# Kernel tuning notes

Hardware: AMD Instinct MI355X
Metric: run time of the kernel (lower is better)

The kernel has to match this reference:

```python
import jax, jax.numpy as jnp
import numpy as np

SIGNAL_SIZE = 33554432  # 2**25
N_ELEMENTS = 25         # log2(SIGNAL_SIZE)


def fft_shift(a, shift):
    # Faithful port of the torch fft_shift (note: 'shift' variable is reused
    # in the original; the phase ramp overwrites it after shift_samples).
    shift = 1.0 - shift
    n_samples = a.shape[-1]
    shift_samples = shift * n_samples * 0.5
    spec = jnp.fft.rfft(a, norm='ortho')
    n_coeffs = spec.shape[-1]
    phase = jnp.arange(n_coeffs) * (2j * np.pi / n_coeffs)  # complex64 ramp
    spec = spec * jnp.exp(phase * shift_samples)
    return jnp.fft.irfft(spec, n=n_samples, norm='ortho')


def setup_inputs() -> dict:
    key = jax.random.key(0)
    elements = jax.random.uniform(key, (N_ELEMENTS,), minval=-1.0, maxval=1.0,
                                  dtype=jnp.float32)
    return {"elements": elements}


def reference(elements):
    # dirac impulse of size 2 at position 0
    signal = jnp.zeros(2, dtype=jnp.float32).at[0].set(1.0)
    for i in range(N_ELEMENTS):  # fixed trip count; sizes double each step
        if i > 0:
            new_signal = jnp.zeros(signal.shape[-1] * 2, dtype=signal.dtype)
            signal = new_signal.at[::2].set(signal)
        shift_factor = 1.0 / (2 ** i)
        signal = fft_shift(signal, elements[i] * shift_factor)
    return signal  # shape [SIGNAL_SIZE]
```

## Files before the change

### kernel.cpp

```cpp
#include <hip/hip_runtime.h>


constexpr float TWOPI_F = 6.28318530717958647692f;
constexpr unsigned M24 = 1u << 24;

__device__ __forceinline__ void phase_sincos(float th, float* sn, float* cs) {
    double d = (double)th * 0.15915494309189533577;
    d -= rint(d);
    float r = (float)d;
    *sn = __builtin_amdgcn_sinf(r);
    *cs = __builtin_amdgcn_cosf(r);
}

__device__ __forceinline__ void sincos_rev(float rev, float* sn, float* cs) {
    float r = rev - rintf(rev);
    *sn = __builtin_amdgcn_sinf(r);
    *cs = __builtin_amdgcn_cosf(r);
}

__device__ __forceinline__ float2 cmul(float2 a, float2 f) {
    return make_float2(a.x * f.x - a.y * f.y, a.x * f.y + a.y * f.x);
}
__device__ __forceinline__ float2 caddf(float2 a, float2 b) { return make_float2(a.x + b.x, a.y + b.y); }
__device__ __forceinline__ float2 csubf(float2 a, float2 b) { return make_float2(a.x - b.x, a.y - b.y); }
__device__ __forceinline__ float2 cmulw(float2 a, float c, float s) {
    return make_float2(a.x * c - a.y * s, a.x * s + a.y * c);
}

__device__ __forceinline__ int xcd_swizzle(int b, int nblocks) {
    int chunk = nblocks >> 3;
    return (b & 7) * chunk + (b >> 3);
}

__device__ __forceinline__ void fft16_inv(float2* v) {
    const float C1 = 0.92387953251128675613f;
    const float S1 = 0.38268343236508977173f;
    const float R2 = 0.70710678118654752440f;
    float2 h[16];
#pragma unroll
    for (int b = 0; b < 4; ++b) {
        float2 s02 = caddf(v[b], v[b + 8]);
        float2 d02 = csubf(v[b], v[b + 8]);
        float2 s13 = caddf(v[b + 4], v[b + 12]);
        float2 d13 = csubf(v[b + 4], v[b + 12]);
        float2 id13 = make_float2(-d13.y, d13.x);
        h[4 * b + 0] = caddf(s02, s13);
        h[4 * b + 1] = caddf(d02, id13);
        h[4 * b + 2] = csubf(s02, s13);
        h[4 * b + 3] = csubf(d02, id13);
    }
    h[5]  = cmulw(h[5],  C1,  S1);
    h[6]  = make_float2(R2 * (h[6].x - h[6].y),  R2 * (h[6].x + h[6].y));
    h[7]  = cmulw(h[7],  S1,  C1);
    h[9]  = make_float2(R2 * (h[9].x - h[9].y),  R2 * (h[9].x + h[9].y));
    h[10] = make_float2(-h[10].y, h[10].x);
    h[11] = cmulw(h[11], -R2, R2);
    h[13] = cmulw(h[13], S1,  C1);
    h[14] = cmulw(h[14], -R2, R2);
    h[15] = cmulw(h[15], -C1, -S1);
#pragma unroll
    for (int K1 = 0; K1 < 4; ++K1) {
        float2 a = h[K1], bb = h[4 + K1], cc = h[8 + K1], dd = h[12 + K1];
        float2 sac = caddf(a, cc), dac = csubf(a, cc);
        float2 sbd = caddf(bb, dd), dbd = csubf(bb, dd);
        float2 idbd = make_float2(-dbd.y, dbd.x);
        v[K1]      = caddf(sac, sbd);
        v[K1 + 4]  = caddf(dac, idbd);
        v[K1 + 8]  = csubf(sac, sbd);
        v[K1 + 12] = csubf(dac, idbd);
    }
}

__device__ __forceinline__ void ztwiddle(float2* v, int q) {
    float ss, cc;
    sincos_rev((float)q * (1.0f / 256.0f), &ss, &cc);
    float2 w = make_float2(1.0f, 0.0f), stp = make_float2(cc, ss);
#pragma unroll
    for (int K1 = 0; K1 < 16; ++K1) {
        v[K1] = cmul(v[K1], w);
        w = cmul(w, stp);
    }
}

__global__ __launch_bounds__(256) void build_q(const float* __restrict__ el,
                                               float2* __restrict__ Q) {
    __shared__ float c_s[18], s_s[18], T_s[18];
    int tid = threadIdx.x;
    if (tid < 18) {
        float e = el[tid];
        float shift1 = e * (1.0f / (float)(1u << tid));
        float sh2 = 1.0f - shift1;
        float s = sh2 * (float)(1u << tid);
        float c = (float)(6.2831853071795864769 / (double)((1u << tid) + 1u));
        c_s[tid] = c;
        s_s[tid] = s;
        float p  = (float)(1u << tid) * c;
        float th = p * s;
        float sn, cs; phase_sincos(th, &sn, &cs);
        T_s[tid] = cs;
    }
    __syncthreads();

    unsigned r = blockIdx.x * 256u + (unsigned)tid;
    if (r == 0u) { Q[0] = make_float2(1.0f, 0.0f); return; }

    unsigned t = (unsigned)__builtin_ctz(r);
    float Pr = T_s[t], Pi = 0.0f;

#pragma unroll
    for (int i = 1; i <= 17; ++i) {
        unsigned hi = 1u << i;
        int sd = (int)((r + hi) & (2u * hi - 1u)) - (int)hi;
        int K  = (i <= (int)t) ? 0 : (sd < 0 ? -sd : sd);
        float sgn = (sd < 0) ? -1.0f : 1.0f;
        float p  = (float)K * c_s[i];
        float th = p * s_s[i];
        float sn, cs; phase_sincos(th, &sn, &cs);
        float ssn = sgn * sn;
        float nr = Pr * cs - Pi * ssn;
        float ni = Pr * ssn + Pi * cs;
        Pr = nr; Pi = ni;
    }
    Q[r] = make_float2(Pr, Pi);
}

__device__ __forceinline__ float2 chain_factor(int i, unsigned k,
                                               const float* __restrict__ c_s,
                                               const float* __restrict__ s_s) {
    unsigned hi = 1u << i;
    int sd = (int)((k + hi) & (2u * hi - 1u)) - (int)hi;
    int K  = (sd < 0) ? -sd : sd;
    float sgn = (sd < 0) ? -1.0f : 1.0f;
    float p  = (float)K * c_s[i];
    float th = p * s_s[i];
    float sn, cs; phase_sincos(th, &sn, &cs);
    return make_float2(cs, sgn * sn);
}

struct WPair { float2 wk, wmk; };

__device__ __forceinline__ WPair chain_tail(unsigned k, float Pr, float Pi,
                                            const float* __restrict__ c_s,
                                            const float* __restrict__ s_s) {
    const float sc = 1.0f / 33554432.0f;
    unsigned mk = M24 - k;
    float thk = ((float)k  * c_s[24]) * s_s[24];
    float thm = ((float)mk * c_s[24]) * s_s[24];
    float snk, csk, snm, csm;
    phase_sincos(thk, &snk, &csk);
    phase_sincos(thm, &snm, &csm);

    float Skr = Pr * csk - Pi * snk;
    float Ski = Pr * snk + Pi * csk;
    float Smr = Pr * csm + Pi * snm;
    float Smi = Pr * snm - Pi * csm;

    float Ar = Skr + Smr, Ai = Ski - Smi;
    float Br = Skr - Smr, Bi = Ski + Smi;
    float ts, tc;
    sincos_rev((float)k * (1.0f / 33554432.0f), &ts, &tc);
    float Cr = tc * Br - ts * Bi;
    float Ci = ts * Br + tc * Bi;

    WPair w;
    w.wk  = make_float2((Ar - Ci) * sc, (Ai + Cr) * sc);
    w.wmk = make_float2((Ar + Ci) * sc, (Cr - Ai) * sc);
    return w;
}

__device__ __forceinline__ WPair chain_W(unsigned k,
                                         const float* __restrict__ c_s,
                                         const float* __restrict__ s_s,
                                         const float* __restrict__ T_s,
                                         const float2* __restrict__ Q) {
    unsigned t = (unsigned)__builtin_ctz(k);
    unsigned r = k & 0x3FFFFu;
    float Pr, Pi;
    if (r != 0u) {
        float2 q = Q[r];
        Pr = q.x; Pi = q.y;
    } else {
        Pr = T_s[t]; Pi = 0.0f;
    }
#pragma unroll
    for (int i = 18; i <= 23; ++i) {
        unsigned hi = 1u << i;
        int sd = (int)((k + hi) & (2u * hi - 1u)) - (int)hi;
        int K  = (i <= (int)t) ? 0 : (sd < 0 ? -sd : sd);
        float sgn = (sd < 0) ? -1.0f : 1.0f;
        float p  = (float)K * c_s[i];
        float th = p * s_s[i];
        float sn, cs; phase_sincos(th, &sn, &cs);
        float ssn = sgn * sn;
        float nr = Pr * cs - Pi * ssn;
        float ni = Pr * ssn + Pi * cs;
        Pr = nr; Pi = ni;
    }
    return chain_tail(k, Pr, Pi, c_s, s_s);
}

__device__ __forceinline__ int c_of_row(int b, int r) {
    if (b == 0) {
        if (r < 8)  return r;
        if (r == 8) return 32768;
        return 65536 - (r - 8);
    }
    return (r < 8) ? (8 * b + r) : (65536 - 8 * b - (r - 8));
}

__global__ __launch_bounds__(256, 4) void fused_build_fft_a(const float* __restrict__ el,
                                                            const float2* __restrict__ Q,
                                                            float2* __restrict__ out) {
    __shared__ float2 lds[16][257];
    __shared__ float c_s[25], s_s[25], T_s[24];
    int tid = threadIdx.x;
    if (tid < 25) {
        float e = el[tid];
        float shift1 = e * (1.0f / (float)(1u << tid));
        float sh2 = 1.0f - shift1;
        float s = sh2 * (float)(1u << tid);
        float c = (float)(6.2831853071795864769 / (double)((1u << tid) + 1u));
        c_s[tid] = c;
        s_s[tid] = s;
        if (tid < 24) {
            float p  = (float)(1u << tid) * c;
            float th = p * s;
            float sn, cs; phase_sincos(th, &sn, &cs);
            T_s[tid] = cs;
        }
    }
    __syncthreads();

    int b = xcd_swizzle(blockIdx.x, 4096);
    int r = tid & 15;
    int q = tid >> 4;
    int c = c_of_row(b, r);
    int rm = (b == 0 && (r == 0 || r == 8)) ? r : (r ^ 8);

    if (b == 0 && r == 0) {
#pragma unroll 1
        for (int u = 0; u < 8; ++u) {
            int k3 = q + 16 * u;
            if (k3 == 0) {
                float p  = 16777216.0f * c_s[24];
                float th = p * s_s[24];
                float sn, cs; phase_sincos(th, &sn, &cs);
                const float sc = 1.0f / 33554432.0f;
                lds[0][0] = make_float2((1.0f + cs) * sc, (1.0f - cs) * sc);
                WPair w = chain_W(8388608u, c_s, s_s, T_s, Q);
                lds[0][128] = w.wk;
            } else {
                unsigned j = (unsigned)k3 << 16;
                WPair w = chain_W(j, c_s, s_s, T_s, Q);
                lds[0][k3] = w.wk;
                lds[0][256 - k3] = w.wmk;
            }
        }
    } else {
        unsigned kbase = (unsigned)c + ((unsigned)q << 16);
        unsigned rres  = kbase & 0x3FFFFu;
        float2 P1 = Q[rres];
        P1 = cmul(P1, chain_factor(18, kbase, c_s, s_s));
        P1 = cmul(P1, chain_factor(19, kbase, c_s, s_s));
        float2 P2[2], P3[4];
#pragma unroll
        for (int j = 0; j < 2; ++j)
            P2[j] = cmul(P1, chain_factor(20, kbase + ((unsigned)j << 20), c_s, s_s));
#pragma unroll
        for (int j = 0; j < 4; ++j)
            P3[j] = cmul(P2[j & 1], chain_factor(21, kbase + ((unsigned)j << 20), c_s, s_s));

#pragma unroll 1
        for (int u = 0; u < 8; ++u) {
            int k3 = q + 16 * u;
            unsigned k = kbase + ((unsigned)u << 20);
            float2 P = cmul(P3[u & 3], chain_factor(22, k, c_s, s_s));
            P = cmul(P, chain_factor(23, k, c_s, s_s));
            WPair w = chain_tail(k, P.x, P.y, c_s, s_s);
            lds[r][k3] = w.wk;
            lds[rm][255 - k3] = w.wmk;
        }
    }
    __syncthreads();

    float2 v[16];
#pragma unroll
    for (int n1 = 0; n1 < 16; ++n1) v[n1] = lds[r][q + 16 * n1];
    fft16_inv(v);
    ztwiddle(v, q);
#pragma unroll
    for (int K1 = 0; K1 < 16; ++K1) lds[r][K1 * 16 + q] = v[K1];
    __syncthreads();

#pragma unroll
    for (int n2 = 0; n2 < 16; ++n2) v[n2] = lds[r][q * 16 + n2];
    fft16_inv(v);
#pragma unroll
    for (int K2 = 0; K2 < 16; ++K2)
        out[c + ((q + 16 * K2) << 16)] = v[K2];
}

__global__ __launch_bounds__(256, 3) void fft_stage_b(const float2* __restrict__ in,
                                                      float2* __restrict__ out) {
    __shared__ float2 lds[16][257];
    int tid = threadIdx.x;
    int wg  = xcd_swizzle(blockIdx.x, 4096);
    int k1b = (wg & 15) * 16;
    int t3  = wg >> 4;
    int row = tid & 15;
    int q   = tid >> 4;

    float2 v[16];
    const float2* src = in + (k1b + row + (q << 8) + (t3 << 16));
#pragma unroll
    for (int u = 0; u < 16; ++u) v[u] = src[u << 12];

    {
        float sb, cb; sincos_rev((float)(t3 * q)  * (1.0f / 65536.0f), &sb, &cb);
        float ssx, csx; sincos_rev((float)t3 * (1.0f / 4096.0f), &ssx, &csx);
        float2 w = make_float2(cb, sb), stp = make_float2(csx, ssx);
#pragma unroll
        for (int u = 0; u < 16; ++u) {
            v[u] = cmul(v[u], w);
            w = cmul(w, stp);
        }
    }
    fft16_inv(v);
    ztwiddle(v, q);
#pragma unroll
    for (int K1 = 0; K1 < 16; ++K1) lds[row][K1 * 16 + q] = v[K1];
    __syncthreads();

#pragma unroll
    for (int n2 = 0; n2 < 16; ++n2) v[n2] = lds[row][q * 16 + n2];
    fft16_inv(v);
#pragma unroll
    for (int K2 = 0; K2 < 16; ++K2)
        out[k1b + row + ((q + 16 * K2) << 8) + (t3 << 16)] = v[K2];
}

__global__ __launch_bounds__(256, 3) void fft_stage_c(const float2* __restrict__ in,
                                                      float2* __restrict__ out) {
    __shared__ float2 lds[16][257];
    int tid = threadIdx.x;
    int wg  = xcd_swizzle(blockIdx.x, 4096);
    int t3b = (wg & 15) * 16;
    int t2  = wg >> 4;

    {
        int k1 = tid;
        const float2* src = in + (k1 + (t2 << 8) + (t3b << 16));
        float2 vb[16];
#pragma unroll
        for (int u = 0; u < 16; ++u) vb[u] = src[u << 16];
        int base = (t3b + (t2 << 8)) * k1;
        float sb, cb; sincos_rev((float)base * (1.0f / 16777216.0f), &sb, &cb);
        float ssx, csx; sincos_rev((float)k1 * (1.0f / 1048576.0f), &ssx, &csx);
        float2 w = make_float2(cb, sb), stp = make_float2(csx, ssx);
#pragma unroll
        for (int u = 0; u < 16; ++u) {
            lds[u][k1] = cmul(vb[u], w);
            w = cmul(w, stp);
        }
    }
    __syncthreads();

    int rr = tid & 15;
    int q  = tid >> 4;
    float2 v[16];
#pragma unroll
    for (int n1 = 0; n1 < 16; ++n1) v[n1] = lds[rr][q + 16 * n1];
    fft16_inv(v);
    ztwiddle(v, q);
#pragma unroll
    for (int K1 = 0; K1 < 16; ++K1) lds[rr][K1 * 16 + q] = v[K1];
    __syncthreads();

#pragma unroll
    for (int n2 = 0; n2 < 16; ++n2) v[n2] = lds[rr][q * 16 + n2];
    fft16_inv(v);
#pragma unroll
    for (int K2 = 0; K2 < 16; ++K2)
        out[(t3b + rr) + (t2 << 8) + ((q + 16 * K2) << 16)] = v[K2];
}

extern "C" void kernel_launch(void* const* d_in, const int* in_sizes, int n_in,
                              void* d_out, int out_size, void* d_ws, size_t ws_size,
                              hipStream_t stream) {
    const float* el = (const float*)d_in[0];
    float2* Gd = (float2*)d_out;
    float2* Q  = (float2*)d_ws;

    hipLaunchKernelGGL(build_q,           dim3(1024), dim3(256), 0, stream, el, Q);
    hipLaunchKernelGGL(fused_build_fft_a, dim3(4096), dim3(256), 0, stream, el, Q, Gd);
    hipLaunchKernelGGL(fft_stage_b,       dim3(4096), dim3(256), 0, stream, Gd, (float2*)d_ws);
    hipLaunchKernelGGL(fft_stage_c,       dim3(4096), dim3(256), 0, stream, (float2*)d_ws, Gd);
}
```

Before: 267.2 us.

## Pair conjugate columns in doubled blocks to share chain factors, drop LDS constant tables

The fused build+FFT-A kernel now uses 512-thread blocks that cover 32 rows: 16 columns plus their conjugate-mirror partners. Each thread's k stride doubles, so one fewer phase-chain factor is recomputed per output and the chain prefix is reused across more outputs. Per-level constants are now computed inline (compile-time constants plus a per-thread recomputation of shifts from the input) instead of staged through shared memory, and the LDS tile uses a rotated indexing to avoid bank conflicts. Larger blocks and more live registers may reduce occupancy.

```diff
diff --git a/kernel.cpp b/kernel.cpp
--- a/kernel.cpp
+++ b/kernel.cpp
@@ -3,6 +3,7 @@
 
 constexpr float TWOPI_F = 6.28318530717958647692f;
 constexpr unsigned M24 = 1u << 24;
+constexpr double TPD = 6.2831853071795864769;
 
 __device__ __forceinline__ void phase_sincos(float th, float* sn, float* cs) {
     double d = (double)th * 0.15915494309189533577;
@@ -30,6 +31,43 @@
 __device__ __forceinline__ int xcd_swizzle(int b, int nblocks) {
     int chunk = nblocks >> 3;
     return (b & 7) * chunk + (b >> 3);
+}
+
+__device__ __forceinline__ float c_of(int i) {
+    switch (i) {
+    case 0:  return (float)(TPD / 2.0);
+    case 1:  return (float)(TPD / 3.0);
+    case 2:  return (float)(TPD / 5.0);
+    case 3:  return (float)(TPD / 9.0);
+    case 4:  return (float)(TPD / 17.0);
+    case 5:  return (float)(TPD / 33.0);
+    case 6:  return (float)(TPD / 65.0);
+    case 7:  return (float)(TPD / 129.0);
+    case 8:  return (float)(TPD / 257.0);
+    case 9:  return (float)(TPD / 513.0);
+    case 10: return (float)(TPD / 1025.0);
+    case 11: return (float)(TPD / 2049.0);
+    case 12: return (float)(TPD / 4097.0);
+    case 13: return (float)(TPD / 8193.0);
+    case 14: return (float)(TPD / 16385.0);
+    case 15: return (float)(TPD / 32769.0);
+    case 16: return (float)(TPD / 65537.0);
+    case 17: return (float)(TPD / 131073.0);
+    case 18: return (float)(TPD / 262145.0);
+    case 19: return (float)(TPD / 524289.0);
+    case 20: return (float)(TPD / 1048577.0);
+    case 21: return (float)(TPD / 2097153.0);
+    case 22: return (float)(TPD / 4194305.0);
+    case 23: return (float)(TPD / 8388609.0);
+    default: return (float)(TPD / 16777217.0);
+    }
+}
+
+__device__ __forceinline__ float s_of(const float* __restrict__ el, int i) {
+    float e = el[i];
+    float shift1 = e * (1.0f / (float)(1u << i));
+    float sh2 = 1.0f - shift1;
+    return sh2 * (float)(1u << i);
 }
 
 __device__ __forceinline__ void fft16_inv(float2* v) {
@@ -124,15 +162,12 @@
     Q[r] = make_float2(Pr, Pi);
 }
 
-__device__ __forceinline__ float2 chain_factor(int i, unsigned k,
-                                               const float* __restrict__ c_s,
-                                               const float* __restrict__ s_s) {
+__device__ __forceinline__ float2 cfac(int i, unsigned k, float ci, float si) {
     unsigned hi = 1u << i;
     int sd = (int)((k + hi) & (2u * hi - 1u)) - (int)hi;
     int K  = (sd < 0) ? -sd : sd;
     float sgn = (sd < 0) ? -1.0f : 1.0f;
-    float p  = (float)K * c_s[i];
-    float th = p * s_s[i];
+    float th = ((float)K * ci) * si;
     float sn, cs; phase_sincos(th, &sn, &cs);
     return make_float2(cs, sgn * sn);
 }
@@ -140,12 +175,11 @@
 struct WPair { float2 wk, wmk; };
 
 __device__ __forceinline__ WPair chain_tail(unsigned k, float Pr, float Pi,
-                                            const float* __restrict__ c_s,
-                                            const float* __restrict__ s_s) {
+                                            float c24, float s24) {
     const float sc = 1.0f / 33554432.0f;
     unsigned mk = M24 - k;
-    float thk = ((float)k  * c_s[24]) * s_s[24];
-    float thm = ((float)mk * c_s[24]) * s_s[24];
+    float thk = ((float)k  * c24) * s24;
+    float thm = ((float)mk * c24) * s24;
     float snk, csk, snm, csm;
     phase_sincos(thk, &snk, &csk);
     phase_sincos(thm, &snm, &csm);
@@ -168,11 +202,8 @@
     return w;
 }
 
-__device__ __forceinline__ WPair chain_W(unsigned k,
-                                         const float* __restrict__ c_s,
-                                         const float* __restrict__ s_s,
-                                         const float* __restrict__ T_s,
-                                         const float2* __restrict__ Q) {
+__device__ WPair chain_W_full(unsigned k, const float* __restrict__ el,
+                              const float2* __restrict__ Q) {
     unsigned t = (unsigned)__builtin_ctz(k);
     unsigned r = k & 0x3FFFFu;
     float Pr, Pi;
@@ -180,7 +211,12 @@
         float2 q = Q[r];
         Pr = q.x; Pi = q.y;
     } else {
-        Pr = T_s[t]; Pi = 0.0f;
+        float ct = c_of((int)t);
+        float st = s_of(el, (int)t);
+        float p  = (float)(1u << t) * ct;
+        float th = p * st;
+        float sn, cs; phase_sincos(th, &sn, &cs);
+        Pr = cs; Pi = 0.0f;
     }
 #pragma unroll
     for (int i = 18; i <= 23; ++i) {
@@ -188,116 +224,107 @@
         int sd = (int)((k + hi) & (2u * hi - 1u)) - (int)hi;
         int K  = (i <= (int)t) ? 0 : (sd < 0 ? -sd : sd);
         float sgn = (sd < 0) ? -1.0f : 1.0f;
-        float p  = (float)K * c_s[i];
-        float th = p * s_s[i];
+        float th = ((float)K * c_of(i)) * s_of(el, i);
         float sn, cs; phase_sincos(th, &sn, &cs);
         float ssn = sgn * sn;
         float nr = Pr * cs - Pi * ssn;
         float ni = Pr * ssn + Pi * cs;
         Pr = nr; Pi = ni;
     }
-    return chain_tail(k, Pr, Pi, c_s, s_s);
-}
-
-__device__ __forceinline__ int c_of_row(int b, int r) {
+    return chain_tail(k, Pr, Pi, c_of(24), s_of(el, 24));
+}
+
+__device__ __forceinline__ int c_of_row32(int b, int r) {
     if (b == 0) {
-        if (r < 8)  return r;
-        if (r == 8) return 32768;
-        return 65536 - (r - 8);
-    }
-    return (r < 8) ? (8 * b + r) : (65536 - 8 * b - (r - 8));
-}
-
-__global__ __launch_bounds__(256, 4) void fused_build_fft_a(const float* __restrict__ el,
+        if (r < 16)  return r;
+        if (r == 16) return 32768;
+        return 65536 - (r - 16);
+    }
+    return (r < 16) ? (16 * b + r) : (65536 - 16 * b - (r - 16));
+}
+
+__global__ __launch_bounds__(512, 4) void fused_build_fft_a(const float* __restrict__ el,
                                                             const float2* __restrict__ Q,
                                                             float2* __restrict__ out) {
-    __shared__ float2 lds[16][257];
-    __shared__ float c_s[25], s_s[25], T_s[24];
+    __shared__ float2 lds2[8192];
+#define LA(r, c_) lds2[(((r) << 8)) | ((((c_) + (r)) & 255))]
     int tid = threadIdx.x;
-    if (tid < 25) {
-        float e = el[tid];
-        float shift1 = e * (1.0f / (float)(1u << tid));
-        float sh2 = 1.0f - shift1;
-        float s = sh2 * (float)(1u << tid);
-        float c = (float)(6.2831853071795864769 / (double)((1u << tid) + 1u));
-        c_s[tid] = c;
-        s_s[tid] = s;
-        if (tid < 24) {
-            float p  = (float)(1u << tid) * c;
-            float th = p * s;
-            float sn, cs; phase_sincos(th, &sn, &cs);
-            T_s[tid] = cs;
-        }
-    }
-    __syncthreads();
-
-    int b = xcd_swizzle(blockIdx.x, 4096);
-    int r = tid & 15;
-    int q = tid >> 4;
-    int c = c_of_row(b, r);
-    int rm = (b == 0 && (r == 0 || r == 8)) ? r : (r ^ 8);
-
-    if (b == 0 && r == 0) {
+    int b  = xcd_swizzle(blockIdx.x, 2048);
+    int pr = tid & 15;
+    int kq = tid >> 4;
+
+    if (b == 0 && pr == 0) {
+        int rsp = (kq < 16) ? 0 : 16;
+        int kql = kq & 15;
+        unsigned cb = (rsp == 0) ? 0u : 32768u;
 #pragma unroll 1
         for (int u = 0; u < 8; ++u) {
-            int k3 = q + 16 * u;
-            if (k3 == 0) {
-                float p  = 16777216.0f * c_s[24];
-                float th = p * s_s[24];
+            int k3 = kql + 16 * u;
+            if (rsp == 0 && k3 == 0) {
+                float c24 = c_of(24), s24v = s_of(el, 24);
+                float th = (16777216.0f * c24) * s24v;
                 float sn, cs; phase_sincos(th, &sn, &cs);
                 const float sc = 1.0f / 33554432.0f;
-                lds[0][0] = make_float2((1.0f + cs) * sc, (1.0f - cs) * sc);
-                WPair w = chain_W(8388608u, c_s, s_s, T_s, Q);
-                lds[0][128] = w.wk;
+                LA(0, 0) = make_float2((1.0f + cs) * sc, (1.0f - cs) * sc);
+                WPair w = chain_W_full(8388608u, el, Q);
+                LA(0, 128) = w.wk;
             } else {
-                unsigned j = (unsigned)k3 << 16;
-                WPair w = chain_W(j, c_s, s_s, T_s, Q);
-                lds[0][k3] = w.wk;
-                lds[0][256 - k3] = w.wmk;
+                unsigned k = cb + ((unsigned)k3 << 16);
+                WPair w = chain_W_full(k, el, Q);
+                if (rsp == 0) { LA(0, k3)  = w.wk; LA(0, 256 - k3)  = w.wmk; }
+                else          { LA(16, k3) = w.wk; LA(16, 255 - k3) = w.wmk; }
             }
         }
     } else {
-        unsigned kbase = (unsigned)c + ((unsigned)q << 16);
+        int c = (b == 0) ? pr : (16 * b + pr);
+        float s18 = s_of(el, 18), s19 = s_of(el, 19), s20 = s_of(el, 20),
+              s21 = s_of(el, 21), s22 = s_of(el, 22), s23 = s_of(el, 23),
+              s24v = s_of(el, 24);
+        unsigned kbase = (unsigned)c + ((unsigned)kq << 16);
         unsigned rres  = kbase & 0x3FFFFu;
         float2 P1 = Q[rres];
-        P1 = cmul(P1, chain_factor(18, kbase, c_s, s_s));
-        P1 = cmul(P1, chain_factor(19, kbase, c_s, s_s));
+        P1 = cmul(P1, cfac(18, kbase, c_of(18), s18));
+        P1 = cmul(P1, cfac(19, kbase, c_of(19), s19));
+        P1 = cmul(P1, cfac(20, kbase, c_of(20), s20));
         float2 P2[2], P3[4];
 #pragma unroll
         for (int j = 0; j < 2; ++j)
-            P2[j] = cmul(P1, chain_factor(20, kbase + ((unsigned)j << 20), c_s, s_s));
+            P2[j] = cmul(P1, cfac(21, kbase + ((unsigned)j << 21), c_of(21), s21));
 #pragma unroll
         for (int j = 0; j < 4; ++j)
-            P3[j] = cmul(P2[j & 1], chain_factor(21, kbase + ((unsigned)j << 20), c_s, s_s));
+            P3[j] = cmul(P2[j & 1], cfac(22, kbase + ((unsigned)j << 21), c_of(22), s22));
 
 #pragma unroll 1
         for (int u = 0; u < 8; ++u) {
-            int k3 = q + 16 * u;
-            unsigned k = kbase + ((unsigned)u << 20);
-            float2 P = cmul(P3[u & 3], chain_factor(22, k, c_s, s_s));
-            P = cmul(P, chain_factor(23, k, c_s, s_s));
-            WPair w = chain_tail(k, P.x, P.y, c_s, s_s);
-            lds[r][k3] = w.wk;
-            lds[rm][255 - k3] = w.wmk;
+            int k3 = kq + 32 * u;
+            unsigned k = kbase + ((unsigned)u << 21);
+            float2 P = cmul(P3[u & 3], cfac(23, k, c_of(23), s23));
+            WPair w = chain_tail(k, P.x, P.y, c_of(24), s24v);
+            LA(pr, k3) = w.wk;
+            LA(pr + 16, 255 - k3) = w.wmk;
         }
     }
     __syncthreads();
 
+    int row = tid & 31;
+    int q   = tid >> 5;
     float2 v[16];
 #pragma unroll
-    for (int n1 = 0; n1 < 16; ++n1) v[n1] = lds[r][q + 16 * n1];
+    for (int n1 = 0; n1 < 16; ++n1) v[n1] = LA(row, q + 16 * n1);
     fft16_inv(v);
     ztwiddle(v, q);
 #pragma unroll
-    for (int K1 = 0; K1 < 16; ++K1) lds[r][K1 * 16 + q] = v[K1];
-    __syncthreads();
-
-#pragma unroll
-    for (int n2 = 0; n2 < 16; ++n2) v[n2] = lds[r][q * 16 + n2];
-    fft16_inv(v);
+    for (int K1 = 0; K1 < 16; ++K1) LA(row, K1 * 16 + q) = v[K1];
+    __syncthreads();
+
+#pragma unroll
+    for (int n2 = 0; n2 < 16; ++n2) v[n2] = LA(row, q * 16 + n2);
+    fft16_inv(v);
+    int cr = c_of_row32(b, row);
 #pragma unroll
     for (int K2 = 0; K2 < 16; ++K2)
-        out[c + ((q + 16 * K2) << 16)] = v[K2];
+        out[cr + ((q + 16 * K2) << 16)] = v[K2];
+#undef LA
 }
 
 __global__ __launch_bounds__(256, 3) void fft_stage_b(const float2* __restrict__ in,
@@ -392,7 +419,7 @@
     float2* Q  = (float2*)d_ws;
 
     hipLaunchKernelGGL(build_q,           dim3(1024), dim3(256), 0, stream, el, Q);
-    hipLaunchKernelGGL(fused_build_fft_a, dim3(4096), dim3(256), 0, stream, el, Q, Gd);
+    hipLaunchKernelGGL(fused_build_fft_a, dim3(2048), dim3(512), 0, stream, el, Q, Gd);
     hipLaunchKernelGGL(fft_stage_b,       dim3(4096), dim3(256), 0, stream, Gd, (float2*)d_ws);
     hipLaunchKernelGGL(fft_stage_c,       dim3(4096), dim3(256), 0, stream, (float2*)d_ws, Gd);
 }
```

New measurement: 255.3 us. 1.05x faster.
